# Kernel optimization log

Hardware: AMD Instinct MI355X
Metric: run time of the kernel (lower is better)

Reference implementation:

```python
import jax, jax.numpy as jnp
import numpy as np

B, S, D = 64, 2048, 512

def setup_inputs() -> dict:
    key = jax.random.key(0)
    k1, k2, k3, k4, k5 = jax.random.split(key, 5)
    x = jax.random.normal(k1, (B, S, D), dtype=jnp.float32)
    # torch Linear(dim, dim): weight [D, D], bias [D]
    W1 = jax.random.normal(k2, (D, D), dtype=jnp.float32) * (1.0 / np.sqrt(D))
    b1 = jax.random.normal(k3, (D,), dtype=jnp.float32) * 0.01
    # torch Linear(dim, 1): weight [1, D] -> stored as [D], bias scalar
    w2 = jax.random.normal(k4, (D,), dtype=jnp.float32) * (1.0 / np.sqrt(D))
    b2 = jax.random.normal(k5, (), dtype=jnp.float32) * 0.01
    return {"x": x, "W1": W1, "b1": b1, "w2": w2, "b2": b2}

def reference(x, W1, b1, w2, b2):
    # score MLP: Linear -> Tanh -> Linear(->1), squeeze
    h = jnp.tanh(jnp.einsum('bsd,ed->bse', x, W1) + b1)   # [B,S,D]
    scores = jnp.einsum('bsd,d->bs', h, w2) + b2          # [B,S]
    w = jax.nn.softmax(scores, axis=1)[..., None]         # [B,S,1]
    ctx = jnp.sum(x * w, axis=1)                          # [B,D]
    return (ctx, w)
```

## Files before the change

### kernel.cpp

```cpp
#include <hip/hip_runtime.h>
#include <hip/hip_bf16.h>

#define BB 64
#define SS 2048
#define DD 512

typedef __attribute__((ext_vector_type(8))) short short8;
typedef __attribute__((ext_vector_type(8))) unsigned short ushort8;
typedef __attribute__((ext_vector_type(4))) float f32x4;

__device__ __forceinline__ unsigned short f2bf(float f){
  union { float f; unsigned int u; } a; a.f = f;
  unsigned int r = a.u + 0x7fffu + ((a.u >> 16) & 1u);
  return (unsigned short)(r >> 16);
}

__device__ __forceinline__ ushort8 pack8(float4 a, float4 b){
  ushort8 u;
  u[0]=f2bf(a.x); u[1]=f2bf(a.y); u[2]=f2bf(a.z); u[3]=f2bf(a.w);
  u[4]=f2bf(b.x); u[5]=f2bf(b.y); u[6]=f2bf(b.z); u[7]=f2bf(b.w);
  return u;
}

__global__ void cvt_w1_kernel(const float* __restrict__ W1, unsigned short* __restrict__ W1b){
  int i = blockIdx.x * blockDim.x + threadIdx.x;
  #pragma unroll
  for (int j = 0; j < 4; ++j){
    int idx = i + j * 65536;
    W1b[idx] = f2bf(W1[idx]);
  }
}

__global__ void zero_ctx_kernel(float* __restrict__ ctx){
  int i = blockIdx.x * blockDim.x + threadIdx.x;
  ctx[i] = 0.f;
}

__launch_bounds__(512, 2)
__global__ void scores_kernel(const float* __restrict__ x,
                              const unsigned short* __restrict__ W1b,
                              const float* __restrict__ b1,
                              const float* __restrict__ w2,
                              float* __restrict__ scores){
  __shared__ __align__(16) unsigned short xs[2][128 * 128];

  const int t    = threadIdx.x;
  const int lane = t & 63;
  const int wv   = t >> 6;
  const int m0   = blockIdx.x * 128;

  f32x4 acc[8][4];
  #pragma unroll
  for (int mt = 0; mt < 8; ++mt)
    #pragma unroll
    for (int et = 0; et < 4; ++et)
      acc[mt][et] = (f32x4){0.f, 0.f, 0.f, 0.f};

  const int srow = t >> 4;
  const int scc  = t & 15;
  const int swz  = (srow & 7) << 4;

  #pragma unroll
  for (int i = 0; i < 4; ++i){
    int row = i * 32 + srow;
    const float* src = x + (size_t)(m0 + row) * DD + scc * 8;
    float4 f0 = *(const float4*)src;
    float4 f1 = *(const float4*)(src + 4);
    *(ushort8*)((char*)&xs[0][0] + row * 256 + ((scc << 4) ^ swz)) = pack8(f0, f1);
  }
  __syncthreads();

  const int arow_off = lane & 15;
  const int kgrp     = lane >> 4;

  #pragma unroll
  for (int p = 0; p < 4; ++p){
    float4 nf[8];
    if (p < 3){
      #pragma unroll
      for (int i = 0; i < 4; ++i){
        int row = i * 32 + srow;
        const float* src = x + (size_t)(m0 + row) * DD + (p + 1) * 128 + scc * 8;
        nf[2*i]   = *(const float4*)src;
        nf[2*i+1] = *(const float4*)(src + 4);
      }
    }
    const char* xb = (const char*)&xs[p & 1][0];
    #pragma unroll
    for (int k8 = 0; k8 < 4; ++k8){
      short8 a[8];
      #pragma unroll
      for (int mt = 0; mt < 8; ++mt){
        int row = mt * 16 + arow_off;
        a[mt] = *(const short8*)(xb + row * 256 + ((k8 * 64 + kgrp * 16) ^ ((row & 7) << 4)));
      }
      short8 bf[4];
      const int ks = p * 4 + k8;
      #pragma unroll
      for (int et = 0; et < 4; ++et){
        int e = (wv << 6) + (et << 4) + arow_off;
        bf[et] = *(const short8*)(W1b + (size_t)e * DD + ks * 32 + kgrp * 8);
      }
      #pragma unroll
      for (int mt = 0; mt < 8; ++mt)
        #pragma unroll
        for (int et = 0; et < 4; ++et)
          acc[mt][et] = __builtin_amdgcn_mfma_f32_16x16x32_bf16(a[mt], bf[et], acc[mt][et], 0, 0, 0);
    }
    if (p < 3){
      #pragma unroll
      for (int i = 0; i < 4; ++i){
        int row = i * 32 + srow;
        *(ushort8*)((char*)&xs[(p + 1) & 1][0] + row * 256 + ((scc << 4) ^ swz)) = pack8(nf[2*i], nf[2*i+1]);
      }
    }
    __syncthreads();
  }

  float ps[8][4];
  #pragma unroll
  for (int mt = 0; mt < 8; ++mt)
    #pragma unroll
    for (int i = 0; i < 4; ++i) ps[mt][i] = 0.f;

  #pragma unroll
  for (int et = 0; et < 4; ++et){
    int e = (wv << 6) + (et << 4) + arow_off;
    float b1v = b1[e];
    float w2v = w2[e];
    #pragma unroll
    for (int mt = 0; mt < 8; ++mt){
      #pragma unroll
      for (int i = 0; i < 4; ++i){
        float g = acc[mt][et][i] + b1v;
        g = fminf(15.f, fmaxf(-15.f, g));
        float ex = __expf(2.f * g);
        float th = 1.f - 2.f / (ex + 1.f);
        ps[mt][i] += th * w2v;
      }
    }
  }
  #pragma unroll
  for (int mt = 0; mt < 8; ++mt)
    #pragma unroll
    for (int i = 0; i < 4; ++i){
      float v = ps[mt][i];
      v += __shfl_xor(v, 1);
      v += __shfl_xor(v, 2);
      v += __shfl_xor(v, 4);
      v += __shfl_xor(v, 8);
      ps[mt][i] = v;
    }
  float* psum = (float*)&xs[0][0];
  if ((lane & 15) == 0){
    #pragma unroll
    for (int mt = 0; mt < 8; ++mt)
      #pragma unroll
      for (int i = 0; i < 4; ++i)
        psum[wv * 128 + mt * 16 + (lane >> 4) * 4 + i] = ps[mt][i];
  }
  __syncthreads();
  if (t < 128){
    float s = 0.f;
    #pragma unroll
    for (int w = 0; w < 8; ++w) s += psum[w * 128 + t];
    scores[m0 + t] = s;
  }
}

__global__ void softmax_kernel(float* __restrict__ wbuf){
  const int b = blockIdx.x;
  float* row = wbuf + (size_t)b * SS;
  const int t = threadIdx.x;
  float v[8];
  #pragma unroll
  for (int i = 0; i < 8; ++i) v[i] = row[t + i * 256];
  float m = v[0];
  #pragma unroll
  for (int i = 1; i < 8; ++i) m = fmaxf(m, v[i]);
  #pragma unroll
  for (int msk = 32; msk >= 1; msk >>= 1) m = fmaxf(m, __shfl_xor(m, msk));
  __shared__ float redm[4], reds[4];
  if ((t & 63) == 0) redm[t >> 6] = m;
  __syncthreads();
  m = fmaxf(fmaxf(redm[0], redm[1]), fmaxf(redm[2], redm[3]));
  float s = 0.f;
  #pragma unroll
  for (int i = 0; i < 8; ++i){ v[i] = __expf(v[i] - m); s += v[i]; }
  #pragma unroll
  for (int msk = 32; msk >= 1; msk >>= 1) s += __shfl_xor(s, msk);
  if ((t & 63) == 0) reds[t >> 6] = s;
  __syncthreads();
  s = reds[0] + reds[1] + reds[2] + reds[3];
  float inv = 1.f / s;
  #pragma unroll
  for (int i = 0; i < 8; ++i) row[t + i * 256] = v[i] * inv;
}

__global__ void ctx_kernel(const float* __restrict__ x, const float* __restrict__ wbuf,
                           float* __restrict__ ctx){
  const int blk = blockIdx.x;
  const int b   = blk >> 4;
  const int sc  = blk & 15;
  const int t   = threadIdx.x;
  const float* xb = x + (size_t)b * SS * DD;
  float a0 = 0.f, a1 = 0.f;
  const int s0 = sc * 128;
  for (int s = s0; s < s0 + 128; ++s){
    float wv = wbuf[(size_t)b * SS + s];
    float2 xv = *(const float2*)(xb + (size_t)s * DD + t * 2);
    a0 += wv * xv.x;
    a1 += wv * xv.y;
  }
  atomicAdd(&ctx[b * DD + t * 2],     a0);
  atomicAdd(&ctx[b * DD + t * 2 + 1], a1);
}

extern "C" void kernel_launch(void* const* d_in, const int* in_sizes, int n_in,
                              void* d_out, int out_size, void* d_ws, size_t ws_size,
                              hipStream_t stream){
  const float* x  = (const float*)d_in[0];
  const float* W1 = (const float*)d_in[1];
  const float* b1 = (const float*)d_in[2];
  const float* w2 = (const float*)d_in[3];

  float* ctx  = (float*)d_out;
  float* wout = (float*)d_out + BB * DD;
  unsigned short* W1b = (unsigned short*)d_ws;

  hipLaunchKernelGGL(cvt_w1_kernel,  dim3(256),  dim3(256), 0, stream, W1, W1b);
  hipLaunchKernelGGL(zero_ctx_kernel,dim3(128),  dim3(256), 0, stream, ctx);
  hipLaunchKernelGGL(scores_kernel,  dim3(1024), dim3(512), 0, stream, x, W1b, b1, w2, wout);
  hipLaunchKernelGGL(softmax_kernel, dim3(64),   dim3(256), 0, stream, wout);
  hipLaunchKernelGGL(ctx_kernel,     dim3(1024), dim3(256), 0, stream, x, wout, ctx);
}
```

Measured before the change: 184.5 us.

## Split score GEMM over E halves, prefetch W1 fragments, replace ctx atomics with partials

Measured after the change: 224.1 us. +21.4%, slower.

```diff
diff --git a/kernel.cpp b/kernel.cpp
--- a/kernel.cpp
+++ b/kernel.cpp
@@ -4,6 +4,7 @@
 #define BB 64
 #define SS 2048
 #define DD 512
+#define MTOT (BB * SS)
 
 typedef __attribute__((ext_vector_type(8))) short short8;
 typedef __attribute__((ext_vector_type(8))) unsigned short ushort8;
@@ -31,27 +32,24 @@
   }
 }
 
-__global__ void zero_ctx_kernel(float* __restrict__ ctx){
-  int i = blockIdx.x * blockDim.x + threadIdx.x;
-  ctx[i] = 0.f;
-}
-
-__launch_bounds__(512, 2)
+__launch_bounds__(256, 3)
 __global__ void scores_kernel(const float* __restrict__ x,
                               const unsigned short* __restrict__ W1b,
                               const float* __restrict__ b1,
                               const float* __restrict__ w2,
-                              float* __restrict__ scores){
-  __shared__ __align__(16) unsigned short xs[2][128 * 128];
+                              float* __restrict__ scorep){
+  __shared__ __align__(16) unsigned short xs[2][64 * 128];
 
   const int t    = threadIdx.x;
   const int lane = t & 63;
   const int wv   = t >> 6;
-  const int m0   = blockIdx.x * 128;
-
-  f32x4 acc[8][4];
-  #pragma unroll
-  for (int mt = 0; mt < 8; ++mt)
+  const int bid  = blockIdx.x;
+  const int ec   = bid & 1;
+  const int m0   = (bid >> 1) * 64;
+
+  f32x4 acc[4][4];
+  #pragma unroll
+  for (int mt = 0; mt < 4; ++mt)
     #pragma unroll
     for (int et = 0; et < 4; ++et)
       acc[mt][et] = (f32x4){0.f, 0.f, 0.f, 0.f};
@@ -60,18 +58,23 @@
   const int scc  = t & 15;
   const int swz  = (srow & 7) << 4;
 
+  const int arow = lane & 15;
+  const int kgrp = lane >> 4;
+  const int ebase = ec * 256 + wv * 64;
+
   #pragma unroll
   for (int i = 0; i < 4; ++i){
-    int row = i * 32 + srow;
+    int row = i * 16 + srow;
     const float* src = x + (size_t)(m0 + row) * DD + scc * 8;
     float4 f0 = *(const float4*)src;
     float4 f1 = *(const float4*)(src + 4);
     *(ushort8*)((char*)&xs[0][0] + row * 256 + ((scc << 4) ^ swz)) = pack8(f0, f1);
   }
-  __syncthreads();
-
-  const int arow_off = lane & 15;
-  const int kgrp     = lane >> 4;
+  short8 bb[2][4];
+  #pragma unroll
+  for (int et = 0; et < 4; ++et)
+    bb[0][et] = *(const short8*)(W1b + (size_t)(ebase + et * 16 + arow) * DD + kgrp * 8);
+  __syncthreads();
 
   #pragma unroll
   for (int p = 0; p < 4; ++p){
@@ -79,7 +82,7 @@
     if (p < 3){
       #pragma unroll
       for (int i = 0; i < 4; ++i){
-        int row = i * 32 + srow;
+        int row = i * 16 + srow;
         const float* src = x + (size_t)(m0 + row) * DD + (p + 1) * 128 + scc * 8;
         nf[2*i]   = *(const float4*)src;
         nf[2*i+1] = *(const float4*)(src + 4);
@@ -88,60 +91,61 @@
     const char* xb = (const char*)&xs[p & 1][0];
     #pragma unroll
     for (int k8 = 0; k8 < 4; ++k8){
-      short8 a[8];
-      #pragma unroll
-      for (int mt = 0; mt < 8; ++mt){
-        int row = mt * 16 + arow_off;
-        a[mt] = *(const short8*)(xb + row * 256 + ((k8 * 64 + kgrp * 16) ^ ((row & 7) << 4)));
-      }
-      short8 bf[4];
       const int ks = p * 4 + k8;
-      #pragma unroll
-      for (int et = 0; et < 4; ++et){
-        int e = (wv << 6) + (et << 4) + arow_off;
-        bf[et] = *(const short8*)(W1b + (size_t)e * DD + ks * 32 + kgrp * 8);
-      }
-      #pragma unroll
-      for (int mt = 0; mt < 8; ++mt)
+      if (ks < 15){
         #pragma unroll
         for (int et = 0; et < 4; ++et)
-          acc[mt][et] = __builtin_amdgcn_mfma_f32_16x16x32_bf16(a[mt], bf[et], acc[mt][et], 0, 0, 0);
+          bb[(ks + 1) & 1][et] = *(const short8*)(W1b + (size_t)(ebase + et * 16 + arow) * DD
+                                                  + (ks + 1) * 32 + kgrp * 8);
+      }
+      short8 a[4];
+      #pragma unroll
+      for (int mt = 0; mt < 4; ++mt){
+        int row = mt * 16 + arow;
+        a[mt] = *(const short8*)(xb + row * 256 + ((k8 * 64 + kgrp * 16) ^ ((row & 7) << 4)));
+      }
+      __builtin_amdgcn_s_setprio(1);
+      #pragma unroll
+      for (int mt = 0; mt < 4; ++mt)
+        #pragma unroll
+        for (int et = 0; et < 4; ++et)
+          acc[mt][et] = __builtin_amdgcn_mfma_f32_16x16x32_bf16(a[mt], bb[ks & 1][et], acc[mt][et], 0, 0, 0);
+      __builtin_amdgcn_s_setprio(0);
     }
     if (p < 3){
       #pragma unroll
       for (int i = 0; i < 4; ++i){
-        int row = i * 32 + srow;
+        int row = i * 16 + srow;
         *(ushort8*)((char*)&xs[(p + 1) & 1][0] + row * 256 + ((scc << 4) ^ swz)) = pack8(nf[2*i], nf[2*i+1]);
       }
     }
     __syncthreads();
   }
 
-  float ps[8][4];
-  #pragma unroll
-  for (int mt = 0; mt < 8; ++mt)
+  float ps[4][4];
+  #pragma unroll
+  for (int mt = 0; mt < 4; ++mt)
     #pragma unroll
     for (int i = 0; i < 4; ++i) ps[mt][i] = 0.f;
 
   #pragma unroll
   for (int et = 0; et < 4; ++et){
-    int e = (wv << 6) + (et << 4) + arow_off;
+    int e = ebase + et * 16 + arow;
     float b1v = b1[e];
     float w2v = w2[e];
     #pragma unroll
-    for (int mt = 0; mt < 8; ++mt){
+    for (int mt = 0; mt < 4; ++mt){
       #pragma unroll
       for (int i = 0; i < 4; ++i){
         float g = acc[mt][et][i] + b1v;
         g = fminf(15.f, fmaxf(-15.f, g));
         float ex = __expf(2.f * g);
-        float th = 1.f - 2.f / (ex + 1.f);
-        ps[mt][i] += th * w2v;
-      }
-    }
-  }
-  #pragma unroll
-  for (int mt = 0; mt < 8; ++mt)
+        ps[mt][i] += (1.f - 2.f / (ex + 1.f)) * w2v;
+      }
+    }
+  }
+  #pragma unroll
+  for (int mt = 0; mt < 4; ++mt)
     #pragma unroll
     for (int i = 0; i < 4; ++i){
       float v = ps[mt][i];
@@ -154,27 +158,27 @@
   float* psum = (float*)&xs[0][0];
   if ((lane & 15) == 0){
     #pragma unroll
-    for (int mt = 0; mt < 8; ++mt)
+    for (int mt = 0; mt < 4; ++mt)
       #pragma unroll
       for (int i = 0; i < 4; ++i)
-        psum[wv * 128 + mt * 16 + (lane >> 4) * 4 + i] = ps[mt][i];
-  }
-  __syncthreads();
-  if (t < 128){
-    float s = 0.f;
-    #pragma unroll
-    for (int w = 0; w < 8; ++w) s += psum[w * 128 + t];
-    scores[m0 + t] = s;
-  }
-}
-
-__global__ void softmax_kernel(float* __restrict__ wbuf){
+        psum[wv * 64 + mt * 16 + (lane >> 4) * 4 + i] = ps[mt][i];
+  }
+  __syncthreads();
+  if (t < 64){
+    float s = psum[t] + psum[64 + t] + psum[128 + t] + psum[192 + t];
+    scorep[(size_t)ec * MTOT + m0 + t] = s;
+  }
+}
+
+__global__ void softmax_kernel(const float* __restrict__ scorep, float* __restrict__ wout){
   const int b = blockIdx.x;
-  float* row = wbuf + (size_t)b * SS;
   const int t = threadIdx.x;
   float v[8];
   #pragma unroll
-  for (int i = 0; i < 8; ++i) v[i] = row[t + i * 256];
+  for (int i = 0; i < 8; ++i){
+    int m = b * SS + t + i * 256;
+    v[i] = scorep[m] + scorep[MTOT + m];
+  }
   float m = v[0];
   #pragma unroll
   for (int i = 1; i < 8; ++i) m = fmaxf(m, v[i]);
@@ -194,26 +198,46 @@
   s = reds[0] + reds[1] + reds[2] + reds[3];
   float inv = 1.f / s;
   #pragma unroll
-  for (int i = 0; i < 8; ++i) row[t + i * 256] = v[i] * inv;
-}
-
-__global__ void ctx_kernel(const float* __restrict__ x, const float* __restrict__ wbuf,
-                           float* __restrict__ ctx){
-  const int blk = blockIdx.x;
-  const int b   = blk >> 4;
-  const int sc  = blk & 15;
+  for (int i = 0; i < 8; ++i) wout[(size_t)b * SS + t + i * 256] = v[i] * inv;
+}
+
+__global__ void ctx_partial_kernel(const float* __restrict__ x, const float* __restrict__ wout,
+                                   float* __restrict__ ctxp){
+  __shared__ float red[4][512];
   const int t   = threadIdx.x;
+  const int sub = t >> 7;
+  const int dt  = t & 127;
+  const int b   = blockIdx.x >> 3;
+  const int sc  = blockIdx.x & 7;
   const float* xb = x + (size_t)b * SS * DD;
-  float a0 = 0.f, a1 = 0.f;
-  const int s0 = sc * 128;
-  for (int s = s0; s < s0 + 128; ++s){
-    float wv = wbuf[(size_t)b * SS + s];
-    float2 xv = *(const float2*)(xb + (size_t)s * DD + t * 2);
-    a0 += wv * xv.x;
-    a1 += wv * xv.y;
-  }
-  atomicAdd(&ctx[b * DD + t * 2],     a0);
-  atomicAdd(&ctx[b * DD + t * 2 + 1], a1);
+  const int s0 = sc * 256 + sub * 64;
+  float4 acc = {0.f, 0.f, 0.f, 0.f};
+  for (int s = s0; s < s0 + 64; ++s){
+    float wv = wout[(size_t)b * SS + s];
+    float4 xv = *(const float4*)(xb + (size_t)s * DD + dt * 4);
+    acc.x += wv * xv.x; acc.y += wv * xv.y; acc.z += wv * xv.z; acc.w += wv * xv.w;
+  }
+  *(float4*)&red[sub][dt * 4] = acc;
+  __syncthreads();
+  if (t < 128){
+    float4 r0 = *(const float4*)&red[0][t * 4];
+    float4 r1 = *(const float4*)&red[1][t * 4];
+    float4 r2 = *(const float4*)&red[2][t * 4];
+    float4 r3 = *(const float4*)&red[3][t * 4];
+    float4 o = { r0.x+r1.x+r2.x+r3.x, r0.y+r1.y+r2.y+r3.y,
+                 r0.z+r1.z+r2.z+r3.z, r0.w+r1.w+r2.w+r3.w };
+    *(float4*)&ctxp[((size_t)(b * 8 + sc)) * DD + t * 4] = o;
+  }
+}
+
+__global__ void ctx_reduce_kernel(const float* __restrict__ ctxp, float* __restrict__ ctx){
+  int i = blockIdx.x * blockDim.x + threadIdx.x;
+  int b = i >> 9;
+  int d = i & 511;
+  float s = 0.f;
+  #pragma unroll
+  for (int sc = 0; sc < 8; ++sc) s += ctxp[((size_t)(b * 8 + sc)) * DD + d];
+  ctx[(size_t)b * DD + d] = s;
 }
 
 extern "C" void kernel_launch(void* const* d_in, const int* in_sizes, int n_in,
@@ -226,11 +250,14 @@
 
   float* ctx  = (float*)d_out;
   float* wout = (float*)d_out + BB * DD;
+
   unsigned short* W1b = (unsigned short*)d_ws;
-
-  hipLaunchKernelGGL(cvt_w1_kernel,  dim3(256),  dim3(256), 0, stream, W1, W1b);
-  hipLaunchKernelGGL(zero_ctx_kernel,dim3(128),  dim3(256), 0, stream, ctx);
-  hipLaunchKernelGGL(scores_kernel,  dim3(1024), dim3(512), 0, stream, x, W1b, b1, w2, wout);
-  hipLaunchKernelGGL(softmax_kernel, dim3(64),   dim3(256), 0, stream, wout);
-  hipLaunchKernelGGL(ctx_kernel,     dim3(1024), dim3(256), 0, stream, x, wout, ctx);
-}
+  float* scorep = (float*)((char*)d_ws + (512u << 10));
+  float* ctxp   = (float*)((char*)d_ws + (512u << 10) + (1024u << 10));
+
+  hipLaunchKernelGGL(cvt_w1_kernel,     dim3(256),  dim3(256), 0, stream, W1, W1b);
+  hipLaunchKernelGGL(scores_kernel,     dim3(4096), dim3(256), 0, stream, x, W1b, b1, w2, scorep);
+  hipLaunchKernelGGL(softmax_kernel,    dim3(64),   dim3(256), 0, stream, scorep, wout);
+  hipLaunchKernelGGL(ctx_partial_kernel,dim3(512),  dim3(512), 0, stream, x, wout, ctxp);
+  hipLaunchKernelGGL(ctx_reduce_kernel, dim3(128),  dim3(256), 0, stream, ctxp, ctx);
+}
```
